# Optimization experiments

Measured on AMD Instinct MI355X. Metric: run time of the kernel, lower is better.

## Reference

```python
import jax, jax.numpy as jnp
import numpy as np

NUM_HEADS = 16
EXP_DIM = 256
HIDDEN = 1024
B, S = 4, 2048


def setup_inputs() -> dict:
    key = jax.random.key(0)
    ks = jax.random.split(key, 16)
    sd = 0.02
    inp = {
        "x": jax.random.normal(ks[0], (B, S, HIDDEN), dtype=jnp.float32),
        "confidence": jax.random.uniform(ks[1], (B,), dtype=jnp.float32),
        "Wq": jax.random.normal(ks[2], (HIDDEN, HIDDEN), dtype=jnp.float32) * sd,
        "bq": jnp.zeros((HIDDEN,), dtype=jnp.float32),
        "Wk": jax.random.normal(ks[3], (HIDDEN, HIDDEN), dtype=jnp.float32) * sd,
        "bk": jnp.zeros((HIDDEN,), dtype=jnp.float32),
        "Wv": jax.random.normal(ks[4], (HIDDEN, HIDDEN), dtype=jnp.float32) * sd,
        "bv": jnp.zeros((HIDDEN,), dtype=jnp.float32),
        "Weq": jax.random.normal(ks[5], (HIDDEN, EXP_DIM), dtype=jnp.float32) * sd,
        "beq": jnp.zeros((EXP_DIM,), dtype=jnp.float32),
        "Wek": jax.random.normal(ks[6], (HIDDEN, EXP_DIM), dtype=jnp.float32) * sd,
        "bek": jnp.zeros((EXP_DIM,), dtype=jnp.float32),
        "Wo": jax.random.normal(ks[7], (HIDDEN, HIDDEN), dtype=jnp.float32) * sd,
        "bo": jnp.zeros((HIDDEN,), dtype=jnp.float32),
    }
    return inp


def reference(x, confidence, Wq, bq, Wk, bk, Wv, bv, Weq, beq, Wek, bek, Wo, bo):
    b, s, h = x.shape
    nh = NUM_HEADS
    hd = h // nh
    # Q/K/V projections -> [B, nh, S, hd]
    q = (x @ Wq + bq).reshape(b, s, nh, hd).transpose(0, 2, 1, 3)
    k = (x @ Wk + bk).reshape(b, s, nh, hd).transpose(0, 2, 1, 3)
    v = (x @ Wv + bv).reshape(b, s, nh, hd).transpose(0, 2, 1, 3)
    scores = jnp.einsum("bhqd,bhkd->bhqk", q, k) / jnp.sqrt(jnp.float32(hd))
    # Experience-based additive bias, confidence-weighted, shared across heads
    exp_q = x @ Weq + beq  # [B, S, E]
    exp_k = x @ Wek + bek  # [B, S, E]
    exp_scores = jnp.einsum("bqe,bke->bqk", exp_q, exp_k) / jnp.sqrt(jnp.float32(EXP_DIM))
    exp_scores = exp_scores * confidence[:, None, None]
    scores = scores + 0.3 * exp_scores[:, None, :, :]
    probs = jax.nn.softmax(scores, axis=-1)  # dropout in eval mode = identity
    ctx = jnp.einsum("bhqk,bhkd->bhqd", probs, v)
    ctx = ctx.transpose(0, 2, 1, 3).reshape(b, s, h)
    return ctx @ Wo + bo
```

## Files before the change

kernel.cpp:

```cpp
#include <hip/hip_runtime.h>

#define HIDDEN 1024
#define EXPD   256
#define NH     16
#define HD     64
#define BB     4
#define SS     2048
#define NTOK   (BB*SS)
#define NCAT   3584
#define QSCALE 0.18033688f

typedef __attribute__((ext_vector_type(8))) short short8;
typedef __attribute__((ext_vector_type(4))) float f32x4;
typedef __attribute__((ext_vector_type(4))) unsigned short us4;

__device__ __forceinline__ unsigned short f2b(float f) {
  unsigned int u = __float_as_uint(f);
  u += 0x7fffu + ((u >> 16) & 1u);
  return (unsigned short)(u >> 16);
}
__device__ __forceinline__ float b2f(unsigned short u) {
  return __uint_as_float(((unsigned int)u) << 16);
}
__device__ __forceinline__ f32x4 mfma_bf16(short8 a, short8 b, f32x4 c) {
  return __builtin_amdgcn_mfma_f32_16x16x32_bf16(a, b, c, 0, 0, 0);
}
__device__ __forceinline__ unsigned int cvt_pk(float lo, float hi) {
  unsigned int r;
  asm("v_cvt_pk_bf16_f32 %0, %1, %2" : "=v"(r) : "v"(lo), "v"(hi));
  return r;
}

__device__ __forceinline__ void gll16(const unsigned short* g, unsigned short* l) {
  __builtin_amdgcn_global_load_lds(
      (const __attribute__((address_space(1))) void*)g,
      (__attribute__((address_space(3))) void*)l, 16, 0, 0);
}

__device__ __forceinline__ short8 lds16(const unsigned short* base, int row, int bx) {
  return *reinterpret_cast<const short8*>(base + row * 64 + ((bx ^ (row & 7)) << 3));
}

__device__ __forceinline__ void stage64(const unsigned short* __restrict__ src,
                                        long long ldg, unsigned short* lds,
                                        int w, int lane) {
#pragma unroll
  for (int t = 0; t < 2; ++t) {
    const int rr = w * 16 + t * 8 + (lane >> 3);
    const int cc = ((lane & 7) ^ (rr & 7)) << 3;
    gll16(src + (long long)rr * ldg + cc, lds + (w * 16 + t * 8) * 64);
  }
}

__device__ __forceinline__ void g2l_call(const unsigned short* __restrict__ g,
                                         long long ldg, unsigned short* lds, int tid) {
  const int r = tid >> 3;
  const int c = ((tid & 7) ^ (r & 7)) << 3;
  gll16(g + (long long)r * ldg + c, lds + (tid >> 6) * 512);
}

__global__ __launch_bounds__(256) void prep_x(const float* __restrict__ x,
                                              unsigned short* __restrict__ A1) {
  const int idx4 = (blockIdx.x * 256 + threadIdx.x) * 4;
  const float4 xv = *reinterpret_cast<const float4*>(&x[idx4]);
  const int token = idx4 >> 10, c = idx4 & 1023;
  float vs[4] = {xv.x, xv.y, xv.z, xv.w};
  unsigned short hi[4], lo[4];
#pragma unroll
  for (int e = 0; e < 4; ++e) {
    unsigned short h = f2b(vs[e]);
    hi[e] = h;
    lo[e] = f2b(vs[e] - b2f(h));
  }
  uint2 hv, lv;
  hv.x = (unsigned int)hi[0] | ((unsigned int)hi[1] << 16);
  hv.y = (unsigned int)hi[2] | ((unsigned int)hi[3] << 16);
  lv.x = (unsigned int)lo[0] | ((unsigned int)lo[1] << 16);
  lv.y = (unsigned int)lo[2] | ((unsigned int)lo[3] << 16);
  *reinterpret_cast<uint2*>(&A1[token * 2048 + c]) = hv;
  *reinterpret_cast<uint2*>(&A1[token * 2048 + 1024 + c]) = lv;
}

__global__ void bias_cat(const float* __restrict__ bq, const float* __restrict__ bk,
                         const float* __restrict__ bv, const float* __restrict__ beq,
                         const float* __restrict__ bek, float* __restrict__ bcat) {
  const int n = blockIdx.x * 256 + threadIdx.x;
  if (n >= NCAT) return;
  float v;
  if (n < 1024) v = bq[n] * QSCALE;
  else if (n < 2048) v = bk[n - 1024];
  else if (n < 3072) v = bv[n - 2048];
  else if (n < 3328) v = beq[n - 3072];
  else v = bek[n - 3328];
  bcat[n] = v;
}

__global__ __launch_bounds__(256) void trans_w(const float* __restrict__ src, int C,
                                               unsigned short* __restrict__ dst, int dstld,
                                               int n_off, int dup, float wscale) {
  __shared__ unsigned short t[64 * 68];
  const int k0 = blockIdx.x * 64, c0 = blockIdx.y * 64;
  const int tid = threadIdx.x;
#pragma unroll
  for (int i = 0; i < 16; ++i) {
    int e = i * 256 + tid;
    int r = e >> 6, c = e & 63;
    t[r * 68 + c] = f2b(src[(k0 + r) * C + c0 + c] * wscale);
  }
  __syncthreads();
#pragma unroll
  for (int i = 0; i < 16; ++i) {
    int e = i * 256 + tid;
    int r2 = e >> 6, c2 = e & 63;
    unsigned short v = t[c2 * 68 + r2];
    dst[(n_off + c0 + r2) * dstld + k0 + c2] = v;
    if (dup) dst[(n_off + c0 + r2) * dstld + 1024 + k0 + c2] = v;
  }
}

__global__ __launch_bounds__(256) void trans_v(const unsigned short* __restrict__ QKVEE,
                                               unsigned short* __restrict__ Vt) {
  __shared__ unsigned short t[64 * 68];
  const int tok0 = blockIdx.x * 64, hc0 = blockIdx.y * 64;
  const int tid = threadIdx.x;
#pragma unroll
  for (int i = 0; i < 16; ++i) {
    int e = i * 256 + tid;
    int r = e >> 6, c = e & 63;
    t[r * 68 + c] = QKVEE[(long long)(tok0 + r) * NCAT + 2048 + hc0 + c];
  }
  __syncthreads();
#pragma unroll
  for (int i = 0; i < 16; ++i) {
    int e = i * 256 + tid;
    int r2 = e >> 6, c2 = e & 63;
    Vt[(long long)(hc0 + r2) * NTOK + tok0 + c2] = t[c2 * 68 + r2];
  }
}

template <int MODE>
__global__ __launch_bounds__(512, 2) void gemm256(
    const unsigned short* __restrict__ A, int lda,
    const unsigned short* __restrict__ Bt, int ldb,
    void* __restrict__ Cv, int ldc,
    const float* __restrict__ bias, int K, int nbn) {
  __shared__ __align__(16) unsigned short As[3 * 256 * 64];
  __shared__ __align__(16) unsigned short Bs[3 * 128 * 64];
  const int tid = threadIdx.x, lane = tid & 63, w8 = tid >> 6;
  int flat = blockIdx.x;
  const int nwg = gridDim.x;
  flat = (flat & 7) * (nwg >> 3) + (flat >> 3);
  const int m0 = (flat / nbn) * 256, n0 = (flat % nbn) * 128;
  const int NT = K >> 6;

  const int R0 = (w8 & 3) * 64, C0 = (w8 >> 2) * 64;
  const int fr = lane & 15, fg = lane >> 4;

  f32x4 acc[4][4];
#pragma unroll
  for (int i = 0; i < 4; ++i)
#pragma unroll
    for (int j = 0; j < 4; ++j)
#pragma unroll
      for (int e = 0; e < 4; ++e) acc[i][j][e] = 0.0f;

#pragma unroll
  for (int p = 0; p < 2; ++p) {
#pragma unroll
    for (int c = 0; c < 4; ++c)
      g2l_call(A + (long long)(m0 + c * 64) * lda + p * 64, lda,
               As + p * 16384 + c * 4096, tid);
#pragma unroll
    for (int c = 0; c < 2; ++c)
      g2l_call(Bt + (long long)(n0 + c * 64) * ldb + p * 64, ldb,
               Bs + p * 8192 + c * 4096, tid);
  }
  asm volatile("s_waitcnt vmcnt(6)" ::: "memory");
  __builtin_amdgcn_s_barrier();
  __builtin_amdgcn_sched_barrier(0);

  int tc = 0, td = 2, ts = 2;
  for (int t = 0; t < NT; ++t) {
    const unsigned short* Ab = As + tc * 16384;
    const unsigned short* Bb = Bs + tc * 8192;
    const int ks0 = ts * 64;
    unsigned short* Ad = As + td * 16384;
    unsigned short* Bd = Bs + td * 8192;

    {
      short8 af[4], bf[4];
#pragma unroll
      for (int mf = 0; mf < 4; ++mf) af[mf] = lds16(Ab, R0 + mf * 16 + fr, fg);
#pragma unroll
      for (int nf = 0; nf < 4; ++nf) bf[nf] = lds16(Bb, C0 + nf * 16 + fr, fg);
#pragma unroll
      for (int c = 0; c < 3; ++c)
        g2l_call(A + (long long)(m0 + c * 64) * lda + ks0, lda, Ad + c * 4096, tid);
      __builtin_amdgcn_s_setprio(1);
#pragma unroll
      for (int mf = 0; mf < 4; ++mf)
#pragma unroll
        for (int nf = 0; nf < 4; ++nf)
          acc[mf][nf] = mfma_bf16(af[mf], bf[nf], acc[mf][nf]);
      __builtin_amdgcn_s_setprio(0);
    }
    {
      short8 af[4], bf[4];
#pragma unroll
      for (int mf = 0; mf < 4; ++mf) af[mf] = lds16(Ab, R0 + mf * 16 + fr, 4 + fg);
#pragma unroll
      for (int nf = 0; nf < 4; ++nf) bf[nf] = lds16(Bb, C0 + nf * 16 + fr, 4 + fg);
      g2l_call(A + (long long)(m0 + 192) * lda + ks0, lda, Ad + 12288, tid);
#pragma unroll
      for (int c = 0; c < 2; ++c)
        g2l_call(Bt + (long long)(n0 + c * 64) * ldb + ks0, ldb, Bd + c * 4096, tid);
      __builtin_amdgcn_s_setprio(1);
#pragma unroll
      for (int mf = 0; mf < 4; ++mf)
#pragma unroll
        for (int nf = 0; nf < 4; ++nf)
          acc[mf][nf] = mfma_bf16(af[mf], bf[nf], acc[mf][nf]);
      __builtin_amdgcn_s_setprio(0);
    }
    asm volatile("s_waitcnt vmcnt(6)" ::: "memory");
    __builtin_amdgcn_s_barrier();
    __builtin_amdgcn_sched_barrier(0);
    tc = (tc == 2) ? 0 : tc + 1;
    td = (td == 2) ? 0 : td + 1;
    ts = (ts + 1 == NT) ? 0 : ts + 1;
  }

  const int rb = m0 + R0 + fg * 4;
  const int cb = n0 + C0 + fr;
#pragma unroll
  for (int mf = 0; mf < 4; ++mf) {
#pragma unroll
    for (int nf = 0; nf < 4; ++nf) {
      const int col = cb + nf * 16;
      const int row0 = rb + mf * 16;
      const float bc = bias[col];
      if (MODE == 0) {
        unsigned short* C = (unsigned short*)Cv;
#pragma unroll
        for (int j = 0; j < 4; ++j)
          C[(long long)(row0 + j) * ldc + col] = f2b(acc[mf][nf][j] + bc);
      } else {
        float* C = (float*)Cv;
#pragma unroll
        for (int j = 0; j < 4; ++j)
          C[(long long)(row0 + j) * ldc + col] = acc[mf][nf][j] + bc;
      }
    }
  }
}

template <int MODE>
__global__ __launch_bounds__(256) void gemm128(
    const unsigned short* __restrict__ A, long long sAz, int lda,
    const unsigned short* __restrict__ Bt, long long sBz, int ldb,
    void* __restrict__ Cv, long long sCz, int ldc,
    const float* __restrict__ bias, const float* __restrict__ cmul,
    float scale, int K) {
  __shared__ __align__(16) unsigned short As[128 * 64];
  __shared__ __align__(16) unsigned short Bs[128 * 64];
  const int tid = threadIdx.x;
  const int lane = tid & 63, w = tid >> 6;
  const int wm = (w >> 1) * 64, wn = (w & 1) * 64;
  int flat = blockIdx.y * gridDim.x + blockIdx.x;
  const int nwg = gridDim.x * gridDim.y;
  flat = (flat & 7) * (nwg >> 3) + (flat >> 3);
  const int m0 = (flat % gridDim.x) * 128, n0 = (flat / gridDim.x) * 128;
  const int z = blockIdx.z;
  A += (long long)z * sAz;
  Bt += (long long)z * sBz;

  f32x4 acc[4][4];
#pragma unroll
  for (int i = 0; i < 4; ++i)
#pragma unroll
    for (int j = 0; j < 4; ++j)
#pragma unroll
      for (int e = 0; e < 4; ++e) acc[i][j][e] = 0.0f;

  const int srow = lane >> 3;
  const int scol = (lane & 7) << 3;

  for (int k0 = 0; k0 < K; k0 += 64) {
#pragma unroll
    for (int t = 0; t < 4; ++t) {
      const int rr = w * 32 + t * 8 + srow;
      gll16(&A[(long long)(m0 + rr) * lda + k0 + scol], &As[(w * 32 + t * 8) * 64]);
      gll16(&Bt[(long long)(n0 + rr) * ldb + k0 + scol], &Bs[(w * 32 + t * 8) * 64]);
    }
    __syncthreads();
#pragma unroll
    for (int kk = 0; kk < 2; ++kk) {
      const int ko = kk * 32 + (lane >> 4) * 8;
      short8 af[4], bf[4];
#pragma unroll
      for (int mf = 0; mf < 4; ++mf)
        af[mf] = *reinterpret_cast<const short8*>(&As[(wm + mf * 16 + (lane & 15)) * 64 + ko]);
#pragma unroll
      for (int nf = 0; nf < 4; ++nf)
        bf[nf] = *reinterpret_cast<const short8*>(&Bs[(wn + nf * 16 + (lane & 15)) * 64 + ko]);
#pragma unroll
      for (int mf = 0; mf < 4; ++mf)
#pragma unroll
        for (int nf = 0; nf < 4; ++nf)
          acc[mf][nf] = mfma_bf16(af[mf], bf[nf], acc[mf][nf]);
    }
    __syncthreads();
  }

  const int rb = m0 + wm + ((lane >> 4) << 2);
  const int cb = n0 + wn + (lane & 15);
  float scl = scale;
  if (MODE == 1) scl *= cmul[z];
#pragma unroll
  for (int mf = 0; mf < 4; ++mf) {
#pragma unroll
    for (int nf = 0; nf < 4; ++nf) {
      const int col = cb + nf * 16;
      const int row0 = rb + mf * 16;
      if (MODE == 1) {
        unsigned short* C = (unsigned short*)Cv + (long long)z * sCz;
        us4 pk;
#pragma unroll
        for (int j = 0; j < 4; ++j) pk[j] = f2b(acc[mf][nf][j] * scl);
        *reinterpret_cast<us4*>(&C[(long long)col * ldc + row0]) = pk;
      }
    }
  }
}

__global__ __launch_bounds__(256, 4) void attn_kernel(
    const unsigned short* __restrict__ QKVEE,
    const unsigned short* __restrict__ Vt,
    const unsigned short* __restrict__ expS,
    unsigned short* __restrict__ ctx) {
  __shared__ __align__(16) unsigned short Ks[64 * 64];
  __shared__ __align__(16) unsigned short Vs[64 * 64];
  __shared__ __align__(16) unsigned short Bs[64 * 64];

  const int tid = threadIdx.x, lane = tid & 63, w = tid >> 6;
  const int flat = blockIdx.x;
  const int pos = flat >> 3;
  const int h = pos & 15, b = (pos >> 4) & 3;
  const int qt = (flat & 7) + 8 * (pos >> 6);
  const int qbase = qt * 64;
  const long long tb = (long long)b * SS;

  const int c0 = lane & 15, g = lane >> 4, r0 = g * 4;
  const int qr = w * 16 + c0;

  short8 qf[2];
#pragma unroll
  for (int kk = 0; kk < 2; ++kk)
    qf[kk] = *reinterpret_cast<const short8*>(
        &QKVEE[(tb + qbase + qr) * NCAT + h * HD + kk * 32 + g * 8]);

  float m = -3.0e38f, l = 0.0f;
  f32x4 acc[4];
#pragma unroll
  for (int nf = 0; nf < 4; ++nf)
#pragma unroll
    for (int j = 0; j < 4; ++j) acc[nf][j] = 0.0f;

  for (int kb = 0; kb < SS; kb += 64) {
    stage64(QKVEE + (tb + kb) * NCAT + HIDDEN + h * HD, NCAT, Ks, w, lane);
    stage64(Vt + (long long)(h * HD) * NTOK + tb + kb, NTOK, Vs, w, lane);
    stage64(expS + (tb + qbase) * SS + kb, SS, Bs, w, lane);
    __syncthreads();

    f32x4 s[4];
#pragma unroll
    for (int nf = 0; nf < 4; ++nf)
#pragma unroll
      for (int j = 0; j < 4; ++j) s[nf][j] = 0.0f;
#pragma unroll
    for (int kk = 0; kk < 2; ++kk) {
      const int bx = kk * 4 + g;
#pragma unroll
      for (int nf = 0; nf < 4; ++nf) {
        short8 kf = lds16(Ks, nf * 16 + c0, bx);
        s[nf] = mfma_bf16(kf, qf[kk], s[nf]);
      }
    }

    float sv[4][4];
#pragma unroll
    for (int nf = 0; nf < 4; ++nf) {
      const int col = nf * 16 + r0;
      const us4 bb = *reinterpret_cast<const us4*>(
          &Bs[qr * 64 + (((col >> 3) ^ (qr & 7)) << 3) + (col & 7)]);
#pragma unroll
      for (int j = 0; j < 4; ++j) sv[nf][j] = s[nf][j] + b2f(bb[j]);
    }

    float t0 = fmaxf(fmaxf(sv[0][0], sv[0][1]), fmaxf(sv[0][2], sv[0][3]));
    float t1 = fmaxf(fmaxf(sv[1][0], sv[1][1]), fmaxf(sv[1][2], sv[1][3]));
    float t2 = fmaxf(fmaxf(sv[2][0], sv[2][1]), fmaxf(sv[2][2], sv[2][3]));
    float t3 = fmaxf(fmaxf(sv[3][0], sv[3][1]), fmaxf(sv[3][2], sv[3][3]));
    float rmax = fmaxf(fmaxf(t0, t1), fmaxf(t2, t3));
    rmax = fmaxf(rmax, __shfl_xor(rmax, 16));
    rmax = fmaxf(rmax, __shfl_xor(rmax, 32));

    if (__any(rmax > m + 8.0f)) {
      const float mn = fmaxf(m, rmax);
      const float sc = __builtin_amdgcn_exp2f(m - mn);
      m = mn;
      l *= sc;
      float scj[4];
#pragma unroll
      for (int j = 0; j < 4; ++j) scj[j] = __shfl(sc, r0 + j);
#pragma unroll
      for (int nf = 0; nf < 4; ++nf)
#pragma unroll
        for (int j = 0; j < 4; ++j) acc[nf][j] *= scj[j];
    }

    unsigned int wds[4][2];
    float ps0 = 0.f, ps1 = 0.f;
#pragma unroll
    for (int nf = 0; nf < 4; ++nf) {
      const float p0 = __builtin_amdgcn_exp2f(sv[nf][0] - m);
      const float p1 = __builtin_amdgcn_exp2f(sv[nf][1] - m);
      const float p2 = __builtin_amdgcn_exp2f(sv[nf][2] - m);
      const float p3 = __builtin_amdgcn_exp2f(sv[nf][3] - m);
      wds[nf][0] = cvt_pk(p0, p1);
      wds[nf][1] = cvt_pk(p2, p3);
      ps0 += p0 + p1;
      ps1 += p2 + p3;
    }
    float psum = ps0 + ps1;
    psum += __shfl_xor(psum, 16);
    psum += __shfl_xor(psum, 32);
    l += psum;

#pragma unroll
    for (int kk = 0; kk < 2; ++kk) {
      union { unsigned int u[4]; short8 v8; } pa;
      pa.u[0] = wds[2 * kk][0];
      pa.u[1] = wds[2 * kk][1];
      pa.u[2] = wds[2 * kk + 1][0];
      pa.u[3] = wds[2 * kk + 1][1];
#pragma unroll
      for (int nf = 0; nf < 4; ++nf) {
        const int rowd = nf * 16 + c0;
        const int cA = kk * 32 + r0;
        const int cB = cA + 16;
        union { us4 h2[2]; short8 v8; } vf;
        vf.h2[0] = *reinterpret_cast<const us4*>(
            &Vs[rowd * 64 + (((cA >> 3) ^ (rowd & 7)) << 3) + (cA & 7)]);
        vf.h2[1] = *reinterpret_cast<const us4*>(
            &Vs[rowd * 64 + (((cB >> 3) ^ (rowd & 7)) << 3) + (cB & 7)]);
        acc[nf] = mfma_bf16(pa.v8, vf.v8, acc[nf]);
      }
    }
    __syncthreads();
  }

  float linv[4];
#pragma unroll
  for (int j = 0; j < 4; ++j) linv[j] = 1.0f / __shfl(l, r0 + j);
#pragma unroll
  for (int nf = 0; nf < 4; ++nf)
#pragma unroll
    for (int j = 0; j < 4; ++j) {
      const int qrow = qbase + w * 16 + r0 + j;
      const int d = nf * 16 + c0;
      ctx[(tb + qrow) * HIDDEN + h * HD + d] = f2b(acc[nf][j] * linv[j]);
    }
}

extern "C" void kernel_launch(void* const* d_in, const int* in_sizes, int n_in,
                              void* d_out, int out_size, void* d_ws, size_t ws_size,
                              hipStream_t stream) {
  const float* x    = (const float*)d_in[0];
  const float* conf = (const float*)d_in[1];
  const float* Wq   = (const float*)d_in[2];
  const float* bq   = (const float*)d_in[3];
  const float* Wk   = (const float*)d_in[4];
  const float* bk   = (const float*)d_in[5];
  const float* Wv   = (const float*)d_in[6];
  const float* bv   = (const float*)d_in[7];
  const float* Weq  = (const float*)d_in[8];
  const float* beq  = (const float*)d_in[9];
  const float* Wek  = (const float*)d_in[10];
  const float* bek  = (const float*)d_in[11];
  const float* Wo   = (const float*)d_in[12];
  const float* bo   = (const float*)d_in[13];

  char* ws = (char*)d_ws;
  unsigned short* A1    = (unsigned short*)(ws);
  unsigned short* WcatT = (unsigned short*)(ws + 33554432);
  float*          bcat  = (float*)(ws + 48234496);
  unsigned short* WoT   = (unsigned short*)(ws + 48250880);
  unsigned short* QKVEE = (unsigned short*)(ws + 50348032);
  unsigned short* Vt    = (unsigned short*)(ws + 109068288);
  unsigned short* ctx   = (unsigned short*)(ws + 125845504);
  unsigned short* expS  = (unsigned short*)d_out;

  prep_x<<<dim3(8192), dim3(256), 0, stream>>>(x, A1);
  bias_cat<<<dim3(14), dim3(256), 0, stream>>>(bq, bk, bv, beq, bek, bcat);
  trans_w<<<dim3(16, 16), dim3(256), 0, stream>>>(Wq, 1024, WcatT, 2048, 0, 1, QSCALE);
  trans_w<<<dim3(16, 16), dim3(256), 0, stream>>>(Wk, 1024, WcatT, 2048, 1024, 1, 1.0f);
  trans_w<<<dim3(16, 16), dim3(256), 0, stream>>>(Wv, 1024, WcatT, 2048, 2048, 1, 1.0f);
  trans_w<<<dim3(16, 4),  dim3(256), 0, stream>>>(Weq, 256, WcatT, 2048, 3072, 1, 1.0f);
  trans_w<<<dim3(16, 4),  dim3(256), 0, stream>>>(Wek, 256, WcatT, 2048, 3328, 1, 1.0f);
  trans_w<<<dim3(16, 16), dim3(256), 0, stream>>>(Wo, 1024, WoT, 1024, 0, 0, 1.0f);

  gemm256<0><<<dim3(896), dim3(512), 0, stream>>>(
      A1, 2048, WcatT, 2048, QKVEE, NCAT, bcat, 2048, 28);

  trans_v<<<dim3(128, 16), dim3(256), 0, stream>>>(QKVEE, Vt);

  gemm128<1><<<dim3(16, 16, 4), dim3(256), 0, stream>>>(
      QKVEE + 3328, (long long)SS * NCAT, NCAT,
      QKVEE + 3072, (long long)SS * NCAT, NCAT,
      expS, (long long)SS * SS, SS, nullptr, conf,
      0.3f * 1.44269504f / 16.0f, 256);

  attn_kernel<<<dim3(2048), dim3(256), 0, stream>>>(QKVEE, Vt, expS, ctx);

  gemm256<2><<<dim3(256), dim3(512), 0, stream>>>(
      ctx, 1024, WoT, 1024, d_out, 1024, bo, 1024, 8);
}
```

Baseline: 476.4 us.

## Fuse V transpose into QKV GEMM epilogue and remap attention blocks per XCD

Measured after the change: 492.3 us. 3.3% more time.

```diff
diff --git a/kernel.cpp b/kernel.cpp
--- a/kernel.cpp
+++ b/kernel.cpp
@@ -118,31 +118,12 @@
   }
 }
 
-__global__ __launch_bounds__(256) void trans_v(const unsigned short* __restrict__ QKVEE,
-                                               unsigned short* __restrict__ Vt) {
-  __shared__ unsigned short t[64 * 68];
-  const int tok0 = blockIdx.x * 64, hc0 = blockIdx.y * 64;
-  const int tid = threadIdx.x;
-#pragma unroll
-  for (int i = 0; i < 16; ++i) {
-    int e = i * 256 + tid;
-    int r = e >> 6, c = e & 63;
-    t[r * 68 + c] = QKVEE[(long long)(tok0 + r) * NCAT + 2048 + hc0 + c];
-  }
-  __syncthreads();
-#pragma unroll
-  for (int i = 0; i < 16; ++i) {
-    int e = i * 256 + tid;
-    int r2 = e >> 6, c2 = e & 63;
-    Vt[(long long)(hc0 + r2) * NTOK + tok0 + c2] = t[c2 * 68 + r2];
-  }
-}
-
 template <int MODE>
 __global__ __launch_bounds__(512, 2) void gemm256(
     const unsigned short* __restrict__ A, int lda,
     const unsigned short* __restrict__ Bt, int ldb,
     void* __restrict__ Cv, int ldc,
+    unsigned short* __restrict__ vt,
     const float* __restrict__ bias, int K, int nbn) {
   __shared__ __align__(16) unsigned short As[3 * 256 * 64];
   __shared__ __align__(16) unsigned short Bs[3 * 128 * 64];
@@ -240,10 +221,17 @@
       const int row0 = rb + mf * 16;
       const float bc = bias[col];
       if (MODE == 0) {
-        unsigned short* C = (unsigned short*)Cv;
-#pragma unroll
-        for (int j = 0; j < 4; ++j)
-          C[(long long)(row0 + j) * ldc + col] = f2b(acc[mf][nf][j] + bc);
+        if (col >= 2048 && col < 3072) {
+          us4 pk;
+#pragma unroll
+          for (int j = 0; j < 4; ++j) pk[j] = f2b(acc[mf][nf][j] + bc);
+          *reinterpret_cast<us4*>(&vt[(long long)(col - 2048) * NTOK + row0]) = pk;
+        } else {
+          unsigned short* C = (unsigned short*)Cv;
+#pragma unroll
+          for (int j = 0; j < 4; ++j)
+            C[(long long)(row0 + j) * ldc + col] = f2b(acc[mf][nf][j] + bc);
+        }
       } else {
         float* C = (float*)Cv;
 #pragma unroll
@@ -333,7 +321,7 @@
   }
 }
 
-__global__ __launch_bounds__(256, 4) void attn_kernel(
+__global__ __launch_bounds__(256, 6) void attn_kernel(
     const unsigned short* __restrict__ QKVEE,
     const unsigned short* __restrict__ Vt,
     const unsigned short* __restrict__ expS,
@@ -344,9 +332,11 @@
 
   const int tid = threadIdx.x, lane = tid & 63, w = tid >> 6;
   const int flat = blockIdx.x;
-  const int pos = flat >> 3;
-  const int h = pos & 15, b = (pos >> 4) & 3;
-  const int qt = (flat & 7) + 8 * (pos >> 6);
+  const int xcd = flat & 7;
+  const int i = flat >> 3;
+  const int qt = i & 31;
+  const int p = xcd * 8 + (i >> 5);
+  const int h = p & 15, b = p >> 4;
   const int qbase = qt * 64;
   const long long tb = (long long)b * SS;
 
@@ -511,9 +501,7 @@
   trans_w<<<dim3(16, 16), dim3(256), 0, stream>>>(Wo, 1024, WoT, 1024, 0, 0, 1.0f);
 
   gemm256<0><<<dim3(896), dim3(512), 0, stream>>>(
-      A1, 2048, WcatT, 2048, QKVEE, NCAT, bcat, 2048, 28);
-
-  trans_v<<<dim3(128, 16), dim3(256), 0, stream>>>(QKVEE, Vt);
+      A1, 2048, WcatT, 2048, QKVEE, NCAT, Vt, bcat, 2048, 28);
 
   gemm128<1><<<dim3(16, 16, 4), dim3(256), 0, stream>>>(
       QKVEE + 3328, (long long)SS * NCAT, NCAT,
@@ -524,5 +512,5 @@
   attn_kernel<<<dim3(2048), dim3(256), 0, stream>>>(QKVEE, Vt, expS, ctx);
 
   gemm256<2><<<dim3(256), dim3(512), 0, stream>>>(
-      ctx, 1024, WoT, 1024, d_out, 1024, bo, 1024, 8);
-}
+      ctx, 1024, WoT, 1024, d_out, 1024, nullptr, bo, 1024, 8);
+}
```
